# Kernel optimization log

Hardware: AMD Instinct MI355X
Metric: run time of the kernel (lower is better)

Reference implementation:

```python
import jax, jax.numpy as jnp
import numpy as np

T = 0.07  # temperature from init default


def _l2norm(x):
    return x / jnp.linalg.norm(x, axis=1, keepdims=True)


def setup_inputs() -> dict:
    key = jax.random.key(0)
    ks = jax.random.split(key, 12)
    B, D, K = 512, 128, 4096
    G = M = 131072
    return {
        "feat": jax.random.normal(ks[0], (B, D), jnp.float32),
        "label": jax.random.randint(ks[1], (B,), 0, 2),
        "out": jnp.zeros((B, K + 1), jnp.float32),   # unused by forward
        "name": jnp.arange(B),                        # unused by forward
        "y": jax.random.randint(ks[2], (B,), 0, G),   # unused by forward
        "memory_feat_gbm": jax.random.normal(ks[3], (G, D), jnp.float32),
        "memory_prob_gbm": jax.random.uniform(ks[4], (G,), jnp.float32),
        "memory_feat_mate": jax.random.normal(ks[5], (M, D), jnp.float32),
        "memory_prob_mate": jax.random.uniform(ks[6], (M,), jnp.float32),
        "idx_n_g": jax.random.randint(ks[7], (K, 1), 0, G),
        "idx_p_g": jax.random.randint(ks[8], (1, 1), 0, G // 4),
        "idx_n_m": jax.random.randint(ks[9], (K, 1), 0, M),
        "idx_p_m": jax.random.randint(ks[10], (1, 1), 0, M // 4),
    }


def reference(feat, label, out, name, y, memory_feat_gbm, memory_prob_gbm,
              memory_feat_mate, memory_prob_mate, idx_n_g, idx_p_g, idx_n_m, idx_p_m):
    # __init__ normalizes the memory banks once
    mfg = _l2norm(memory_feat_gbm)
    mfm = _l2norm(memory_feat_mate)
    feat_n = _l2norm(feat)  # [B, D]
    output_size = mfg.shape[0]

    # gather positive / negative prototypes (all rows unit-norm, so
    # cosine_similarity == dot product)
    wp_g = mfg[idx_p_g.ravel()]   # [1, D]
    wn_g = mfg[idx_n_g.ravel()]   # [K, D]
    wp_m = mfm[idx_p_m.ravel()]   # [1, D]
    wn_m = mfm[idx_n_m.ravel()]   # [K, D]

    # label==0 (gbm): pos from gbm bank, negs from mate bank; label==1 mirrored
    row_gbm = jnp.concatenate([feat_n @ wp_g.T, feat_n @ wn_m.T], axis=1)   # [B, K+1]
    row_mate = jnp.concatenate([feat_n @ wp_m.T, feat_n @ wn_g.T], axis=1)  # [B, K+1]
    sims = jnp.where((label == 0)[:, None], row_gbm, row_mate)

    # use_softmax=False path: exp(s/T) / Z with Z set from first batch (treated as constant)
    e = jnp.exp(sims / T)
    Z = jax.lax.stop_gradient(e.mean() * output_size)
    out_feature_p_n = e / Z

    # confident cluster members + current batch (data-dependent sizes; eager jax)
    mask_g = memory_prob_gbm > 0.5
    mask_m = memory_prob_mate > 0.6
    feature_clu_all = jnp.concatenate([mfg[mask_g], mfm[mask_m], feat_n], axis=0)
    gt_clu_all = jnp.concatenate([
        jnp.zeros((int(mask_g.sum()),), label.dtype),
        jnp.ones((int(mask_m.sum()),), label.dtype),
        label,
    ], axis=0)
    return out_feature_p_n, feature_clu_all, gt_clu_all
```

## Files before the change

kernel.cpp:

```cpp
#include <hip/hip_runtime.h>
#include <math.h>


#define TINV 14.2857142857142857f
#define JT 64
#define BT2 64

typedef __attribute__((ext_vector_type(8))) short bfrag;
typedef __attribute__((ext_vector_type(4))) float ffrag;
typedef __attribute__((ext_vector_type(4))) float f4v;

__device__ __forceinline__ float wredsum64(float v) {
#pragma unroll
  for (int m = 32; m > 0; m >>= 1) v += __shfl_xor(v, m, 64);
  return v;
}

__device__ __forceinline__ int wredsum64i(int v) {
#pragma unroll
  for (int m = 32; m > 0; m >>= 1) v += __shfl_xor(v, m, 64);
  return v;
}

__device__ __forceinline__ unsigned short f2bf(float x) {
  unsigned u = __float_as_uint(x);
  u += 0x7fffu + ((u >> 16) & 1u);
  return (unsigned short)(u >> 16);
}

__device__ __forceinline__ bfrag ldsread(const short* base, int row, int kb) {
  return *(const bfrag*)((const char*)base + row * 256 +
                         (kb ^ ((row & 7) << 4)));
}
__device__ __forceinline__ void ldswrite(short* base, int row, int kb,
                                         bfrag v) {
  *(bfrag*)((char*)base + row * 256 + (kb ^ ((row & 7) << 4))) = v;
}

__global__ __launch_bounds__(256) void k_stageA(
    const float* __restrict__ feat, const int* __restrict__ label,
    const float* __restrict__ mfg, const float* __restrict__ pg,
    const float* __restrict__ mfm, const float* __restrict__ pm,
    const int* __restrict__ idxpg, const int* __restrict__ idxpm,
    float* __restrict__ outp, long long cluTail, long long gtTail,
    int* __restrict__ bucket, int* __restrict__ n0p,
    int* __restrict__ cg64, int* __restrict__ cm64,
    float* __restrict__ posPartials,
    int B, int K1, int G, int M,
    int nCountBlk, int nFeatBlk, int nPosBlk) {
  int bid = blockIdx.x, t = threadIdx.x;

  if (bid < nCountBlk) {
    int i = bid * 256 + t;
    int a = (i < G) && (pg[i] > 0.5f);
    int b = (i < M) && (pm[i] > 0.6f);
    unsigned long long ba = __ballot(a), bb = __ballot(b);
    int lane = t & 63, w = t >> 6;
    if (lane == 0) {
      cg64[bid * 4 + w] = __popcll(ba);
      cm64[bid * 4 + w] = __popcll(bb);
    }
    return;
  }
  bid -= nCountBlk;

  if (bid < nFeatBlk) {
    int gid = bid * 256 + t;
    int w = gid >> 6, lane = gid & 63;
    if (w < B) {
      float2 v = ((const float2*)feat)[(long long)w * 64 + lane];
      float sq = wredsum64(v.x * v.x + v.y * v.y);
      float inv = rsqrtf(sq);
      ((float2*)(outp + cluTail))[(long long)w * 64 + lane] =
          make_float2(v.x * inv, v.y * inv);
      if (lane == 0) outp[gtTail + w] = (float)label[w];
    }
    return;
  }
  bid -= nFeatBlk;

  if (bid < nPosBlk) {
    __shared__ float ps[4];
    int gid = bid * 256 + t;
    int w = gid >> 6, lane = gid & 63, lw = t >> 6;
    float e = 0.f;
    if (w < B) {
      int lab = label[w];
      const float* bank = lab ? mfm : mfg;
      long long row = lab ? idxpm[0] : idxpg[0];
      float2 wv = ((const float2*)(bank + row * 128))[lane];
      float2 fv = ((const float2*)feat)[(long long)w * 64 + lane];
      float dot = wredsum64(fv.x * wv.x + fv.y * wv.y);
      float sqw = wredsum64(wv.x * wv.x + wv.y * wv.y);
      float sqf = wredsum64(fv.x * fv.x + fv.y * fv.y);
      e = expf(dot * rsqrtf(sqw) * rsqrtf(sqf) * TINV);
      if (lane == 0) outp[(long long)w * K1] = e;
    }
    if (lane == 0) ps[lw] = e;
    __syncthreads();
    if (t == 0) posPartials[bid] = ps[0] + ps[1] + ps[2] + ps[3];
    return;
  }

  {
    __shared__ int sc[512];
    int t2 = t + 256;
    int m0 = (t < B) ? (label[t] == 0 ? 1 : 0) : 0;
    int m1 = (t2 < B) ? (label[t2] == 0 ? 1 : 0) : 0;
    sc[t] = m0; sc[t2] = m1;
    __syncthreads();
    for (int off = 1; off < 512; off <<= 1) {
      int u0 = (t >= off) ? sc[t - off] : 0;
      int u1 = (t2 >= off) ? sc[t2 - off] : 0;
      __syncthreads();
      sc[t] += u0; sc[t2] += u1;
      __syncthreads();
    }
    int n0 = (B > 0) ? sc[B - 1] : 0;
    if (t < B) {
      int incl = sc[t];
      if (m0) bucket[incl - 1] = t; else bucket[n0 + t - incl] = t;
    }
    if (t2 < B) {
      int incl = sc[t2];
      if (m1) bucket[incl - 1] = t2; else bucket[n0 + t2 - incl] = t2;
    }
    if (t == 0) *n0p = n0;
  }
}

__global__ __launch_bounds__(256) void k_stageB(
    const float* __restrict__ featn, const int* __restrict__ bucket,
    const int* __restrict__ n0ptr,
    const float* __restrict__ mfg, const float* __restrict__ mfm,
    const float* __restrict__ pg, const float* __restrict__ pm,
    const int* __restrict__ idxng, const int* __restrict__ idxnm,
    const int* __restrict__ cg64, const int* __restrict__ cm64,
    float* __restrict__ out0, float* __restrict__ partials,
    int* __restrict__ rowlist, float* __restrict__ outp, long long gtBase,
    int B, int K, int K1, int G, int M, int NG64, int simsGx, int nSimsBlk) {
  int t = threadIdx.x;

  if ((int)blockIdx.x >= nSimsBlk) {
    __shared__ int red[4];
    int gb = (int)blockIdx.x - nSimsBlk;
    int bankId = gb / NG64;
    int g = gb - bankId * NG64;
    const float* probs = bankId ? pm : pg;
    float thr = bankId ? 0.6f : 0.5f;
    int Nelem = bankId ? M : G;
    int lane = t & 63, w = t >> 6;

    int s = 0;
    for (int j = t; j < NG64; j += 256) {
      if (bankId == 0) {
        if (j < g) s += cg64[j];
      } else {
        s += cg64[j];
        if (j < g) s += cm64[j];
      }
    }
    s = wredsum64i(s);
    if (lane == 0) red[w] = s;
    __syncthreads();
    if (t < 64) {
      long long off = (long long)red[0] + red[1] + red[2] + red[3];
      int c = g * 64 + t;
      int f = (c < Nelem) && (probs[c] > thr);
      unsigned long long mb = __ballot(f);
      unsigned long long below = t ? ((~0ull) >> (64 - t)) : 0ull;
      if (f) {
        long long dst = off + __popcll(mb & below);
        rowlist[dst] = c | (bankId << 24);
        outp[gtBase + dst] = (float)bankId;
      }
    }
    return;
  }

  __shared__ __align__(16) short wlds[64 * 128];
  __shared__ __align__(16) short flds[64 * 128];
  __shared__ float invw[64];
  __shared__ float bs[4];
  int pidx = (int)blockIdx.x;
  int bx = pidx % simsGx, by = pidx / simsGx;
  int n0 = *n0ptr;
  int nb0 = (n0 + BT2 - 1) / BT2;
  int lab, p0, cnt;
  if (by < nb0) {
    lab = 0; p0 = by * BT2; cnt = min(BT2, n0 - p0);
  } else {
    int k = by - nb0; p0 = n0 + k * BT2;
    int n1 = B - n0; cnt = min(BT2, n1 - k * BT2); lab = 1;
  }
  if (cnt <= 0) { if (t == 0) partials[pidx] = 0.f; return; }
  const float* bank = lab == 0 ? mfm : mfg;
  const int* idxN   = lab == 0 ? idxnm : idxng;
  int j0 = bx * JT;

#pragma unroll
  for (int q = 0; q < 4; q++) {
    int slot = q * 256 + t;
    int row = slot >> 4, ch = slot & 15;
    long long srow = idxN[j0 + row];
    const float4* gp = (const float4*)(bank + srow * 128 + ch * 8);
    float4 x0 = gp[0], x1 = gp[1];
    bfrag h;
    h[0] = (short)f2bf(x0.x); h[1] = (short)f2bf(x0.y);
    h[2] = (short)f2bf(x0.z); h[3] = (short)f2bf(x0.w);
    h[4] = (short)f2bf(x1.x); h[5] = (short)f2bf(x1.y);
    h[6] = (short)f2bf(x1.z); h[7] = (short)f2bf(x1.w);
    ldswrite(wlds, row, ch * 16, h);
    float s = x0.x*x0.x + x0.y*x0.y + x0.z*x0.z + x0.w*x0.w +
              x1.x*x1.x + x1.y*x1.y + x1.z*x1.z + x1.w*x1.w;
    s += __shfl_xor(s, 1, 64);
    s += __shfl_xor(s, 2, 64);
    s += __shfl_xor(s, 4, 64);
    s += __shfl_xor(s, 8, 64);
    if (ch == 0) invw[row] = rsqrtf(s);
  }
#pragma unroll
  for (int q = 0; q < 4; q++) {
    int slot = q * 256 + t;
    int row = slot >> 4, ch = slot & 15;
    bfrag h;
#pragma unroll
    for (int i = 0; i < 8; i++) h[i] = 0;
    if (row < cnt) {
      int bg = bucket[p0 + row];
      const float4* gp = (const float4*)(featn + (long long)bg * 128 + ch * 8);
      float4 x0 = gp[0], x1 = gp[1];
      h[0] = (short)f2bf(x0.x); h[1] = (short)f2bf(x0.y);
      h[2] = (short)f2bf(x0.z); h[3] = (short)f2bf(x0.w);
      h[4] = (short)f2bf(x1.x); h[5] = (short)f2bf(x1.y);
      h[6] = (short)f2bf(x1.z); h[7] = (short)f2bf(x1.w);
    }
    ldswrite(flds, row, ch * 16, h);
  }
  __syncthreads();

  int l = t & 63, wv = t >> 6;
  int wj = wv & 1, wb = wv >> 1;
  int colb = l & 15, kg = l >> 4;
  ffrag acc00 = {0.f, 0.f, 0.f, 0.f};
  ffrag acc01 = {0.f, 0.f, 0.f, 0.f};
  ffrag acc10 = {0.f, 0.f, 0.f, 0.f};
  ffrag acc11 = {0.f, 0.f, 0.f, 0.f};
#pragma unroll
  for (int ks = 0; ks < 4; ks++) {
    int kb = ks * 64 + kg * 16;
    bfrag a0 = ldsread(flds, wb * 32 + colb,      kb);
    bfrag a1 = ldsread(flds, wb * 32 + 16 + colb, kb);
    bfrag b0 = ldsread(wlds, wj * 32 + colb,      kb);
    bfrag b1 = ldsread(wlds, wj * 32 + 16 + colb, kb);
    acc00 = __builtin_amdgcn_mfma_f32_16x16x32_bf16(a0, b0, acc00, 0, 0, 0);
    acc01 = __builtin_amdgcn_mfma_f32_16x16x32_bf16(a0, b1, acc01, 0, 0, 0);
    acc10 = __builtin_amdgcn_mfma_f32_16x16x32_bf16(a1, b0, acc10, 0, 0, 0);
    acc11 = __builtin_amdgcn_mfma_f32_16x16x32_bf16(a1, b1, acc11, 0, 0, 0);
  }

  float mysum = 0.f;
  int rowg = l >> 4;
  auto epi = [&](const ffrag& A, int bt, int jt) {
    int bl = wb * 32 + bt * 16 + rowg * 4;
    int jl = wj * 32 + jt * 16 + colb;
    float iw = invw[jl];
#pragma unroll
    for (int r = 0; r < 4; r++) {
      int b2 = bl + r;
      if (b2 < cnt) {
        int bg = bucket[p0 + b2];
        float e = expf(A[r] * iw * TINV);
        out0[(long long)bg * K1 + 1 + j0 + jl] = e;
        mysum += e;
      }
    }
  };
  epi(acc00, 0, 0); epi(acc01, 0, 1); epi(acc10, 1, 0); epi(acc11, 1, 1);

  float wsum = wredsum64(mysum);
  if ((t & 63) == 0) bs[t >> 6] = wsum;
  __syncthreads();
  if (t == 0) partials[pidx] = bs[0] + bs[1] + bs[2] + bs[3];
}

__global__ __launch_bounds__(256) void k_stageD(
    const float* __restrict__ mfg, const float* __restrict__ mfm,
    const int* __restrict__ rowlist,
    float* __restrict__ outp, long long cluBase, int nSel, int nGatherBlk,
    float* __restrict__ out0, const float* __restrict__ partials, int nPart,
    double factor, long long n4) {
  int t = threadIdx.x;

  if ((int)blockIdx.x < nGatherBlk) {
    __shared__ int rl[32];
    int base = (int)blockIdx.x * 32;
    if (t < 32) {
      int d = base + t;
      rl[t] = (d < nSel) ? rowlist[d] : 0;
    }
    __syncthreads();
    int hw = t >> 5, l = t & 31;
#pragma unroll
    for (int k = 0; k < 2; k++) {
      int r0 = hw * 4 + k * 2, r1 = r0 + 1;
      if (base + r0 < nSel) {
        bool h1 = (base + r1) < nSel;
        int e0 = rl[r0];
        int e1 = rl[h1 ? r1 : r0];
        const float* p0 = ((e0 >> 24) ? mfm : mfg) +
                          (long long)(e0 & 0xFFFFFF) * 128;
        const float* p1 = ((e1 >> 24) ? mfm : mfg) +
                          (long long)(e1 & 0xFFFFFF) * 128;
        f4v v0 = *(const f4v*)(p0 + l * 4);
        f4v v1 = *(const f4v*)(p1 + l * 4);
        float q0 = v0.x * v0.x + v0.y * v0.y + v0.z * v0.z + v0.w * v0.w;
        float q1 = v1.x * v1.x + v1.y * v1.y + v1.z * v1.z + v1.w * v1.w;
#pragma unroll
        for (int m = 16; m > 0; m >>= 1) {
          q0 += __shfl_xor(q0, m, 64);
          q1 += __shfl_xor(q1, m, 64);
        }
        float i0 = rsqrtf(q0), i1 = rsqrtf(q1);
        f4v o0 = {v0.x * i0, v0.y * i0, v0.z * i0, v0.w * i0};
        *(f4v*)(outp + cluBase + (long long)(base + r0) * 128 + l * 4) = o0;
        if (h1) {
          f4v o1 = {v1.x * i1, v1.y * i1, v1.z * i1, v1.w * i1};
          *(f4v*)(outp + cluBase + (long long)(base + r1) * 128 + l * 4) = o1;
        }
      }
    }
    return;
  }

  __shared__ double sd[256];
  double s = 0.0;
  for (int i = t; i < nPart; i += 256) s += (double)partials[i];
  sd[t] = s;
  __syncthreads();
  for (int off = 128; off > 0; off >>= 1) {
    if (t < off) sd[t] += sd[t + off];
    __syncthreads();
  }
  float sc = (float)(factor / sd[0]);
  long long bb = (long long)((int)blockIdx.x - nGatherBlk) * 256 + t;
  long long stride = (long long)(gridDim.x - nGatherBlk) * 256;
  for (long long i = bb; i < n4; i += stride) {
    float4 v = ((float4*)out0)[i];
    v.x *= sc; v.y *= sc; v.z *= sc; v.w *= sc;
    ((float4*)out0)[i] = v;
  }
}

extern "C" void kernel_launch(void* const* d_in, const int* in_sizes, int n_in,
                              void* d_out, int out_size, void* d_ws,
                              size_t ws_size, hipStream_t stream) {
  const float* feat  = (const float*)d_in[0];
  const int*   label = (const int*)d_in[1];
  const float* mfg   = (const float*)d_in[5];
  const float* pg    = (const float*)d_in[6];
  const float* mfm   = (const float*)d_in[7];
  const float* pm    = (const float*)d_in[8];
  const int*   idxng = (const int*)d_in[9];
  const int*   idxpg = (const int*)d_in[10];
  const int*   idxnm = (const int*)d_in[11];
  const int*   idxpm = (const int*)d_in[12];
  float* outp = (float*)d_out;

  const int B = in_sizes[1];
  const int D = 128;
  const int K = in_sizes[9];
  const int G = in_sizes[6];
  const int M = in_sizes[8];
  const int K1 = K + 1;

  const long long C0 = (long long)B * K1;
  const long long R = ((long long)out_size - C0) / (D + 1);
  const long long G0 = C0 + R * D;
  const long long cluTail = C0 + (R - B) * (long long)D;
  const long long gtTail = G0 + (R - B);
  const int nSel = (int)(R - B);

  const float* featn = outp + cluTail;

  char* wsb = (char*)d_ws;
  size_t o = 0;
  auto alloc = [&](size_t bytes) -> char* {
    char* p = wsb + o;
    o = (o + bytes + 255) & ~(size_t)255;
    return p;
  };
  const int simsGx = K / JT;
  const int simsGy = B / BT2 + 2;
  const int nPartSims = simsGx * simsGy;
  const int nPosBlk = (B * 64 + 255) / 256;
  float* partials = (float*)alloc(sizeof(float) * (nPartSims + nPosBlk));
  int* bucket = (int*)alloc(sizeof(int) * B);
  int* n0p = (int*)alloc(sizeof(int) * 4);
  const int NB = ((G > M ? G : M) + 255) / 256;
  const int NG64 = NB * 4;
  int* cg64 = (int*)alloc(sizeof(int) * NG64);
  int* cm64 = (int*)alloc(sizeof(int) * NG64);
  int* rowlist = (int*)alloc(sizeof(int) * (size_t)nSel);
  (void)ws_size; (void)n_in;

  const int nFeatBlk = (B * 64 + 255) / 256;
  const int gridA = NB + nFeatBlk + nPosBlk + 1;
  const int nEmitBlk = 2 * NG64;
  const int gridB = nPartSims + nEmitBlk;
  const int nGatherBlk = (nSel + 31) / 32;
  const int nScaleBlk = 512;
  const int gridD = nGatherBlk + nScaleBlk;

  k_stageA<<<gridA, 256, 0, stream>>>(
      feat, label, mfg, pg, mfm, pm, idxpg, idxpm,
      outp, cluTail, gtTail, bucket, n0p, cg64, cm64,
      partials + nPartSims, B, K1, G, M, NB, nFeatBlk, nPosBlk);

  k_stageB<<<gridB, 256, 0, stream>>>(
      featn, bucket, n0p, mfg, mfm, pg, pm, idxng, idxnm,
      cg64, cm64, outp, partials, rowlist, outp, G0,
      B, K, K1, G, M, NG64, simsGx, nPartSims);

  double factor = (double)B * (double)K1 / (double)G;
  k_stageD<<<gridD, 256, 0, stream>>>(
      mfg, mfm, rowlist, outp, C0, nSel, nGatherBlk,
      outp, partials, nPartSims + nPosBlk, factor, C0 / 4);
}
```

Before: 52.13 us.

## Precompute inverse norms of selected rows in stage A, simplify stage D copy

Adds norm blocks to stage A that compact the confident rows of each bank, compute their inverse L2 norms and store them in a workspace array. Stage D then does a flat scaled copy with one float4 per thread, reading the precomputed inverse norm, with no shuffle reductions on the tail path. The aim is to move the norm reduction earlier, where it overlaps with other stage-A work, and to shorten the final kernel. The cost is that the selected rows are read twice from global memory (once in A, once in D), plus an extra workspace array of G+M floats.

```diff
diff --git a/kernel.cpp b/kernel.cpp
--- a/kernel.cpp
+++ b/kernel.cpp
@@ -45,10 +45,64 @@
     float* __restrict__ outp, long long cluTail, long long gtTail,
     int* __restrict__ bucket, int* __restrict__ n0p,
     int* __restrict__ cg64, int* __restrict__ cm64,
-    float* __restrict__ posPartials,
-    int B, int K1, int G, int M,
-    int nCountBlk, int nFeatBlk, int nPosBlk) {
+    float* __restrict__ invn_cand, float* __restrict__ posPartials,
+    int B, int K1, int G, int M, int NG64,
+    int nNormBlk, int nCountBlk, int nFeatBlk, int nPosBlk) {
   int bid = blockIdx.x, t = threadIdx.x;
+
+  if (bid < nNormBlk) {
+    __shared__ int selRow[64];
+    __shared__ int Ssh;
+    int bankId = bid / NG64;
+    int g = bid - bankId * NG64;
+    const float* probs = bankId ? pm : pg;
+    const float* rows  = bankId ? mfm : mfg;
+    float thr = bankId ? 0.6f : 0.5f;
+    int Nelem = bankId ? M : G;
+    if (t < 64) {
+      int c = g * 64 + t;
+      int f = (c < Nelem) && (probs[c] > thr);
+      unsigned long long mb = __ballot(f);
+      unsigned long long below = t ? ((~0ull) >> (64 - t)) : 0ull;
+      if (f) selRow[__popcll(mb & below)] = c;
+      if (t == 0) Ssh = (int)__popcll(mb);
+    }
+    __syncthreads();
+    int S = Ssh;
+    if (S == 0) return;
+    float* invdst = invn_cand + (long long)bankId * G;
+    int hw = t >> 5, l = t & 31;
+    for (int r0 = hw * 4; r0 < S; r0 += 32) {
+      int ra = r0;
+      int rb = min(r0 + 1, S - 1);
+      int rc = min(r0 + 2, S - 1);
+      int rd = min(r0 + 3, S - 1);
+      int sa = selRow[ra], sb = selRow[rb], sc2 = selRow[rc], sd2 = selRow[rd];
+      f4v v0 = *(const f4v*)(rows + (long long)sa * 128 + l * 4);
+      f4v v1 = *(const f4v*)(rows + (long long)sb * 128 + l * 4);
+      f4v v2 = *(const f4v*)(rows + (long long)sc2 * 128 + l * 4);
+      f4v v3 = *(const f4v*)(rows + (long long)sd2 * 128 + l * 4);
+      float q0 = v0.x * v0.x + v0.y * v0.y + v0.z * v0.z + v0.w * v0.w;
+      float q1 = v1.x * v1.x + v1.y * v1.y + v1.z * v1.z + v1.w * v1.w;
+      float q2 = v2.x * v2.x + v2.y * v2.y + v2.z * v2.z + v2.w * v2.w;
+      float q3 = v3.x * v3.x + v3.y * v3.y + v3.z * v3.z + v3.w * v3.w;
+#pragma unroll
+      for (int m = 16; m > 0; m >>= 1) {
+        q0 += __shfl_xor(q0, m, 64);
+        q1 += __shfl_xor(q1, m, 64);
+        q2 += __shfl_xor(q2, m, 64);
+        q3 += __shfl_xor(q3, m, 64);
+      }
+      if (l == 0) {
+        invdst[sa] = rsqrtf(q0);
+        if (r0 + 1 < S) invdst[sb] = rsqrtf(q1);
+        if (r0 + 2 < S) invdst[sc2] = rsqrtf(q2);
+        if (r0 + 3 < S) invdst[sd2] = rsqrtf(q3);
+      }
+    }
+    return;
+  }
+  bid -= nNormBlk;
 
   if (bid < nCountBlk) {
     int i = bid * 256 + t;
@@ -286,49 +340,26 @@
 
 __global__ __launch_bounds__(256) void k_stageD(
     const float* __restrict__ mfg, const float* __restrict__ mfm,
-    const int* __restrict__ rowlist,
-    float* __restrict__ outp, long long cluBase, int nSel, int nGatherBlk,
+    const int* __restrict__ rowlist, const float* __restrict__ invn_cand,
+    float* __restrict__ outp, long long cluBase, int nSel, int G,
+    int nCopyBlk,
     float* __restrict__ out0, const float* __restrict__ partials, int nPart,
     double factor, long long n4) {
   int t = threadIdx.x;
 
-  if ((int)blockIdx.x < nGatherBlk) {
-    __shared__ int rl[32];
-    int base = (int)blockIdx.x * 32;
-    if (t < 32) {
-      int d = base + t;
-      rl[t] = (d < nSel) ? rowlist[d] : 0;
-    }
-    __syncthreads();
-    int hw = t >> 5, l = t & 31;
-#pragma unroll
-    for (int k = 0; k < 2; k++) {
-      int r0 = hw * 4 + k * 2, r1 = r0 + 1;
-      if (base + r0 < nSel) {
-        bool h1 = (base + r1) < nSel;
-        int e0 = rl[r0];
-        int e1 = rl[h1 ? r1 : r0];
-        const float* p0 = ((e0 >> 24) ? mfm : mfg) +
-                          (long long)(e0 & 0xFFFFFF) * 128;
-        const float* p1 = ((e1 >> 24) ? mfm : mfg) +
-                          (long long)(e1 & 0xFFFFFF) * 128;
-        f4v v0 = *(const f4v*)(p0 + l * 4);
-        f4v v1 = *(const f4v*)(p1 + l * 4);
-        float q0 = v0.x * v0.x + v0.y * v0.y + v0.z * v0.z + v0.w * v0.w;
-        float q1 = v1.x * v1.x + v1.y * v1.y + v1.z * v1.z + v1.w * v1.w;
-#pragma unroll
-        for (int m = 16; m > 0; m >>= 1) {
-          q0 += __shfl_xor(q0, m, 64);
-          q1 += __shfl_xor(q1, m, 64);
-        }
-        float i0 = rsqrtf(q0), i1 = rsqrtf(q1);
-        f4v o0 = {v0.x * i0, v0.y * i0, v0.z * i0, v0.w * i0};
-        *(f4v*)(outp + cluBase + (long long)(base + r0) * 128 + l * 4) = o0;
-        if (h1) {
-          f4v o1 = {v1.x * i1, v1.y * i1, v1.z * i1, v1.w * i1};
-          *(f4v*)(outp + cluBase + (long long)(base + r1) * 128 + l * 4) = o1;
-        }
-      }
+  if ((int)blockIdx.x < nCopyBlk) {
+    int flat = (int)blockIdx.x * 256 + t;
+    int total = nSel * 32;
+    if (flat < total) {
+      int row = flat >> 5, c = flat & 31;
+      int e = rowlist[row];
+      int src = e & 0xFFFFFF;
+      int bk = e >> 24;
+      const float* bp = bk ? mfm : mfg;
+      float iw = invn_cand[(long long)bk * G + src];
+      f4v v = *(const f4v*)(bp + (long long)src * 128 + c * 4);
+      f4v o = {v.x * iw, v.y * iw, v.z * iw, v.w * iw};
+      *(f4v*)(outp + cluBase + (long long)row * 128 + c * 4) = o;
     }
     return;
   }
@@ -343,8 +374,8 @@
     __syncthreads();
   }
   float sc = (float)(factor / sd[0]);
-  long long bb = (long long)((int)blockIdx.x - nGatherBlk) * 256 + t;
-  long long stride = (long long)(gridDim.x - nGatherBlk) * 256;
+  long long bb = (long long)((int)blockIdx.x - nCopyBlk) * 256 + t;
+  long long stride = (long long)(gridDim.x - nCopyBlk) * 256;
   for (long long i = bb; i < n4; i += stride) {
     float4 v = ((float4*)out0)[i];
     v.x *= sc; v.y *= sc; v.z *= sc; v.w *= sc;
@@ -402,20 +433,23 @@
   int* cg64 = (int*)alloc(sizeof(int) * NG64);
   int* cm64 = (int*)alloc(sizeof(int) * NG64);
   int* rowlist = (int*)alloc(sizeof(int) * (size_t)nSel);
+  float* invn_cand = (float*)alloc(sizeof(float) * (size_t)(G + M));
   (void)ws_size; (void)n_in;
 
   const int nFeatBlk = (B * 64 + 255) / 256;
-  const int gridA = NB + nFeatBlk + nPosBlk + 1;
+  const int nNormBlk = 2 * NG64;
+  const int gridA = nNormBlk + NB + nFeatBlk + nPosBlk + 1;
   const int nEmitBlk = 2 * NG64;
   const int gridB = nPartSims + nEmitBlk;
-  const int nGatherBlk = (nSel + 31) / 32;
+  const int nCopyBlk = (nSel * 32 + 255) / 256;
   const int nScaleBlk = 512;
-  const int gridD = nGatherBlk + nScaleBlk;
+  const int gridD = nCopyBlk + nScaleBlk;
 
   k_stageA<<<gridA, 256, 0, stream>>>(
       feat, label, mfg, pg, mfm, pm, idxpg, idxpm,
-      outp, cluTail, gtTail, bucket, n0p, cg64, cm64,
-      partials + nPartSims, B, K1, G, M, NB, nFeatBlk, nPosBlk);
+      outp, cluTail, gtTail, bucket, n0p, cg64, cm64, invn_cand,
+      partials + nPartSims, B, K1, G, M, NG64,
+      nNormBlk, NB, nFeatBlk, nPosBlk);
 
   k_stageB<<<gridB, 256, 0, stream>>>(
       featn, bucket, n0p, mfg, mfm, pg, pm, idxng, idxnm,
@@ -424,6 +458,6 @@
 
   double factor = (double)B * (double)K1 / (double)G;
   k_stageD<<<gridD, 256, 0, stream>>>(
-      mfg, mfm, rowlist, outp, C0, nSel, nGatherBlk,
+      mfg, mfm, rowlist, invn_cand, outp, C0, nSel, G, nCopyBlk,
       outp, partials, nPartSims + nPosBlk, factor, C0 / 4);
 }
```

Measured after the change: 59.38 us. 1.14x slower.
